# Performance work log

Hardware: AMD Instinct MI355X
Metric: run time of the kernel (lower is better)

The kernel has to match this reference:

```python
import jax, jax.numpy as jnp
import numpy as np

B, S, F = 2, 2048, 2048
H, D = 16, 128  # F == H * D


def setup_inputs() -> dict:
    key = jax.random.key(0)
    k1, k2, k3 = jax.random.split(key, 3)
    x = jax.random.normal(k1, (B, S, F), dtype=jnp.float32)
    # causal attention mask, broadcast over batch and heads
    mask = jnp.tril(jnp.ones((S, S), dtype=bool))[None, None, :, :]
    init_std = 0.02
    c_attn_kernel = jax.random.normal(k2, (F, 3 * F), dtype=jnp.float32) * init_std
    c_attn_bias = jnp.zeros((3 * F,), dtype=jnp.float32)
    c_proj_kernel = jax.random.normal(k3, (F, F), dtype=jnp.float32) * init_std
    c_proj_bias = jnp.zeros((F,), dtype=jnp.float32)
    return {
        "x": x,
        "mask": mask,
        "c_attn_kernel": c_attn_kernel,
        "c_attn_bias": c_attn_bias,
        "c_proj_kernel": c_proj_kernel,
        "c_proj_bias": c_proj_bias,
    }


def reference(x, mask, c_attn_kernel, c_attn_bias, c_proj_kernel, c_proj_bias):
    dtype = x.dtype
    # fused QKV projection: [B,S,F] @ [F,3F] -> [B,S,3F]
    hidden = jnp.einsum('bsf,fe->bse', x, c_attn_kernel) + c_attn_bias
    q, k, v = jnp.split(hidden, 3, axis=-1)
    split = lambda t: t.reshape(t.shape[:-1] + (H, D))  # [B,S,H,D]
    q, k, v = split(q), split(k), split(v)
    q = q / jnp.sqrt(jnp.asarray(D, dtype))
    scores = jnp.einsum('bqhd,bkhd->bhqk', q, k)  # [B,H,S,S]
    big_neg = jnp.finfo(dtype).min
    scores = jnp.where(mask[..., :S, :S], scores, big_neg)
    weights = jax.nn.softmax(scores, axis=-1)
    z = jnp.einsum('bhqk,bkhd->bqhd', weights, v)  # [B,S,H,D]
    merged = z.reshape(z.shape[:-2] + (F,))  # [B,S,F]
    out = jnp.einsum('bsf,fe->bse', merged, c_proj_kernel) + c_proj_bias
    return out
```

## Files before the change

### kernel.cpp

```cpp
#include <hip/hip_runtime.h>
#include <hip/hip_bf16.h>
#include <stdint.h>

typedef __attribute__((ext_vector_type(8))) __bf16 bf16x8;
typedef __attribute__((ext_vector_type(4))) __bf16 bf16x4;
typedef __attribute__((ext_vector_type(4))) float f32x4;

#define DEV __device__ __forceinline__

static constexpr int S = 2048, F = 2048, H = 16, D = 128;
static constexpr int KDIM = F;
static constexpr float QSCALE = 0.08838834764831845f;

DEV void gll16(const void* g, void* l) {
  __builtin_amdgcn_global_load_lds(
      (const __attribute__((address_space(1))) void*)g,
      (__attribute__((address_space(3))) void*)l, 16, 0, 0);
}

DEV f32x4 mfma16(bf16x8 a, bf16x8 b, f32x4 c) {
  return __builtin_amdgcn_mfma_f32_16x16x32_bf16(a, b, c, 0, 0, 0);
}

extern __shared__ char smem[];

__global__ void k_prep(const float* __restrict__ x, __bf16* __restrict__ xb,
                       const float* __restrict__ wa, __bf16* __restrict__ wat,
                       const float* __restrict__ wp, __bf16* __restrict__ wpt) {
  __shared__ float t[64][65];
  const int bid = blockIdx.x;
  if (bid < 8192) {
    int i = bid * 256 + threadIdx.x;
    float4 v = reinterpret_cast<const float4*>(x)[i];
    bf16x4 o = {(__bf16)v.x, (__bf16)v.y, (__bf16)v.z, (__bf16)v.w};
    reinterpret_cast<bf16x4*>(xb)[i] = o;
    return;
  }
  const float* in;
  __bf16* out;
  int rows, cols, c0, r0;
  if (bid < 11264) {
    int tb = bid - 8192;
    in = wa; out = wat; rows = 2048; cols = 6144;
    c0 = (tb % 96) * 64; r0 = (tb / 96) * 64;
  } else {
    int tb = bid - 11264;
    in = wp; out = wpt; rows = 2048; cols = 2048;
    c0 = (tb % 32) * 64; r0 = (tb / 32) * 64;
  }
  const int tx = threadIdx.x & 63, ty = threadIdx.x >> 6;
#pragma unroll
  for (int i = 0; i < 64; i += 4)
    t[ty + i][tx] = in[(size_t)(r0 + ty + i) * cols + c0 + tx];
  __syncthreads();
#pragma unroll
  for (int i = 0; i < 64; i += 4)
    out[(size_t)(c0 + ty + i) * rows + r0 + tx] = (__bf16)t[tx][ty + i];
}

template <int BM, int BN, int NBXL, int EPI>
__global__ __launch_bounds__(512, 1) void k_gp(
    const __bf16* __restrict__ A, const __bf16* __restrict__ Bt,
    const float* __restrict__ bias,
    __bf16* __restrict__ qo, __bf16* __restrict__ ko, __bf16* __restrict__ vo,
    float* __restrict__ fo) {
  constexpr int MF = BM / 32;
  constexpr int NF = BN / 64;
  constexpr int NH = NF / 2;
  constexpr int NLA = BM / 64;
  constexpr int NLB = BN / 64;
  constexpr int NL = NLA + NLB;
  constexpr int AOFF = BM * 128;
  constexpr int BUFSZ = (BM + BN) * 128;
  constexpr int NT = KDIM / 64;

  const int tid = threadIdx.x;
  const int lane = tid & 63, wid = tid >> 6;
  const int wm = wid >> 2, wn = wid & 3;
  const int ln = lane & 15, lm = lane >> 4;

  const int q8 = gridDim.x >> 3;
  const int lin = (blockIdx.x & 7) * q8 + (blockIdx.x >> 3);
  const int by = lin >> NBXL, bx = lin & ((1 << NBXL) - 1);
  const int mBase = by * BM, nBase = bx * BN;

  const int r0 = tid >> 3, cc = tid & 7;
  const int src0 = r0 * KDIM + ((cc ^ (r0 & 7)) << 3);
  const __bf16* Ab = A + (size_t)mBase * KDIM + src0;
  const __bf16* Bb = Bt + (size_t)nBase * KDIM + src0;
  const int dstBase = wid * 1024;

  auto stage = [&](char* buf, int t) {
    const __bf16* As = Ab + t * 64;
    const __bf16* Bs = Bb + t * 64;
#pragma unroll
    for (int j = 0; j < NLA; ++j)
      gll16(As + (size_t)j * 64 * KDIM, buf + j * 8192 + dstBase);
#pragma unroll
    for (int j = 0; j < NLB; ++j)
      gll16(Bs + (size_t)j * 64 * KDIM, buf + AOFF + j * 8192 + dstBase);
  };
  auto wait_nl = [&]() {
    if constexpr (NL == 4)       asm volatile("s_waitcnt vmcnt(4)" ::: "memory");
    else if constexpr (NL == 6)  asm volatile("s_waitcnt vmcnt(6)" ::: "memory");
    else if constexpr (NL == 8)  asm volatile("s_waitcnt vmcnt(8)" ::: "memory");
    else                         asm volatile("s_waitcnt vmcnt(10)" ::: "memory");
  };

  int rA[2], rB[2];
#pragma unroll
  for (int ks = 0; ks < 2; ++ks) {
    const int slot = (ks * 4 + lm) ^ (ln & 7);
    rA[ks] = (wm * (BM / 2) + ln) * 128 + slot * 16;
    rB[ks] = AOFF + (wn * (BN / 4) + ln) * 128 + slot * 16;
  }

  f32x4 acc[MF][NF] = {};

  stage(smem, 0);
  stage(smem + BUFSZ, 1);
  wait_nl();
  __builtin_amdgcn_s_barrier();
  __builtin_amdgcn_sched_barrier(0);

  for (int t = 0; t < NT; ++t) {
    char* cb = smem + (t & 1) * BUFSZ;
    bf16x8 a0[MF], a1[MF], b0[NF], b1[NF];

#pragma unroll
    for (int mi = 0; mi < MF; ++mi)
      a0[mi] = *reinterpret_cast<const bf16x8*>(cb + rA[0] + mi * 2048);
#pragma unroll
    for (int ni = 0; ni < NH; ++ni)
      b0[ni] = *reinterpret_cast<const bf16x8*>(cb + rB[0] + ni * 2048);
#pragma unroll
    for (int ni = NH; ni < NF; ++ni)
      b0[ni] = *reinterpret_cast<const bf16x8*>(cb + rB[0] + ni * 2048);

    __builtin_amdgcn_s_setprio(1);
#pragma unroll
    for (int ni = 0; ni < NH; ++ni)
#pragma unroll
      for (int mi = 0; mi < MF; ++mi)
        acc[mi][ni] = mfma16(a0[mi], b0[ni], acc[mi][ni]);
    __builtin_amdgcn_s_setprio(0);

#pragma unroll
    for (int mi = 0; mi < MF; ++mi)
      a1[mi] = *reinterpret_cast<const bf16x8*>(cb + rA[1] + mi * 2048);
#pragma unroll
    for (int ni = NH; ni < NF; ++ni)
      b1[ni] = *reinterpret_cast<const bf16x8*>(cb + rB[1] + ni * 2048);

    __builtin_amdgcn_s_setprio(1);
#pragma unroll
    for (int ni = NH; ni < NF; ++ni)
#pragma unroll
      for (int mi = 0; mi < MF; ++mi)
        acc[mi][ni] = mfma16(a0[mi], b0[ni], acc[mi][ni]);
    __builtin_amdgcn_s_setprio(0);

#pragma unroll
    for (int ni = 0; ni < NH; ++ni)
      b1[ni] = *reinterpret_cast<const bf16x8*>(cb + rB[1] + ni * 2048);

    __builtin_amdgcn_s_setprio(1);
#pragma unroll
    for (int ni = NH; ni < NF; ++ni)
#pragma unroll
      for (int mi = 0; mi < MF; ++mi)
        acc[mi][ni] = mfma16(a1[mi], b1[ni], acc[mi][ni]);
    __builtin_amdgcn_s_setprio(0);

    asm volatile("s_waitcnt lgkmcnt(0)" ::: "memory");
    __builtin_amdgcn_s_barrier();
    __builtin_amdgcn_sched_barrier(0);
    if (t + 2 < NT) stage(cb, t + 2);

    __builtin_amdgcn_s_setprio(1);
#pragma unroll
    for (int ni = 0; ni < NH; ++ni)
#pragma unroll
      for (int mi = 0; mi < MF; ++mi)
        acc[mi][ni] = mfma16(a1[mi], b1[ni], acc[mi][ni]);
    __builtin_amdgcn_s_setprio(0);

    if (t + 2 < NT) {
      wait_nl();
    } else if (t + 1 < NT) {
      asm volatile("s_waitcnt vmcnt(0)" ::: "memory");
    }
    if (t + 1 < NT) {
      __builtin_amdgcn_s_barrier();
      __builtin_amdgcn_sched_barrier(0);
    }
  }

  if (EPI == 0) {
#pragma unroll
    for (int mi = 0; mi < MF; ++mi) {
      const int grow = mBase + wm * (BM / 2) + mi * 16 + lm * 4;
      const int b = grow >> 11, s0 = grow & 2047;
#pragma unroll
      for (int ni = 0; ni < NF; ++ni) {
        const int gcol = nBase + wn * (BN / 4) + ni * 16 + ln;
        const float bv = bias[gcol];
        const int sec = gcol >> 11;
        const int h = (gcol >> 7) & 15, d = gcol & 127;
        const int bh = b * H + h;
        if (sec == 0) {
#pragma unroll
          for (int r = 0; r < 4; ++r)
            qo[((size_t)bh * S + s0 + r) * D + d] = (__bf16)((acc[mi][ni][r] + bv) * QSCALE);
        } else if (sec == 1) {
#pragma unroll
          for (int r = 0; r < 4; ++r)
            ko[((size_t)bh * S + s0 + r) * D + d] = (__bf16)(acc[mi][ni][r] + bv);
        } else {
          bf16x4 pv = {(__bf16)(acc[mi][ni][0] + bv), (__bf16)(acc[mi][ni][1] + bv),
                       (__bf16)(acc[mi][ni][2] + bv), (__bf16)(acc[mi][ni][3] + bv)};
          *reinterpret_cast<bf16x4*>(vo + ((size_t)bh * D + d) * S + s0) = pv;
        }
      }
    }
  } else {
#pragma unroll
    for (int mi = 0; mi < MF; ++mi) {
      const int grow = mBase + wm * (BM / 2) + mi * 16 + lm * 4;
#pragma unroll
      for (int ni = 0; ni < NF; ++ni) {
        const int gcol = nBase + wn * (BN / 4) + ni * 16 + ln;
        const float bv = bias[gcol];
#pragma unroll
        for (int r = 0; r < 4; ++r)
          fo[(size_t)(grow + r) * F + gcol] = acc[mi][ni][r] + bv;
      }
    }
  }
}

__global__ __launch_bounds__(256, 2) void k_attn(
    const __bf16* __restrict__ qb, const __bf16* __restrict__ kb,
    const __bf16* __restrict__ vtb, __bf16* __restrict__ zb) {
  const int lane = threadIdx.x & 63, w = threadIdx.x >> 6;
  const int lm = lane >> 4, ln = lane & 15;
  const int blk = blockIdx.x;
  const int u = blk & 255, v = blk >> 8;
  const int qt = v ? (u >> 4) : 15 - (u >> 4);
  const int bh = ((u & 15) << 1) | v;
  const int qw = qt * 128 + w * 32;

  const __bf16* qp = qb + (size_t)bh * S * D;
  const __bf16* kp = kb + (size_t)bh * S * D;
  const __bf16* vp = vtb + (size_t)bh * D * S;
  char* pw = smem + 65536 + w * 4096;

  int ksrc[4], kdst[4], vsrc[4], vdst[4];
#pragma unroll
  for (int j = 0; j < 4; ++j) {
    int c = (w * 4 + j) * 64 + lane;
    int kr = c >> 4, kps = (c & 15) ^ (kr & 7);
    ksrc[j] = kr * D + kps * 8;
    kdst[j] = (w * 4 + j) * 1024;
    int vr = c >> 3, vps = (c & 7) ^ (vr & 7);
    vsrc[j] = vr * S + vps * 8;
    vdst[j] = 16384 + (w * 4 + j) * 1024;
  }
  auto stage = [&](int kt) {
    char* buf = smem + (kt & 1) * 32768;
    const int kv = kt * 64;
#pragma unroll
    for (int j = 0; j < 4; ++j) gll16(kp + (size_t)kv * D + ksrc[j], buf + kdst[j]);
#pragma unroll
    for (int j = 0; j < 4; ++j) gll16(vp + kv + vsrc[j], buf + vdst[j]);
  };

  bf16x8 qf[2][4];
#pragma unroll
  for (int mi = 0; mi < 2; ++mi)
#pragma unroll
    for (int kf = 0; kf < 4; ++kf)
      qf[mi][kf] = *reinterpret_cast<const bf16x8*>(qp + (qw + mi * 16 + ln) * D + kf * 32 + lm * 8);

  f32x4 Oa[2][8] = {};
  float mrow[2][4], lrow[2][4];
#pragma unroll
  for (int mi = 0; mi < 2; ++mi)
#pragma unroll
    for (int r = 0; r < 4; ++r) { mrow[mi][r] = -3.0e38f; lrow[mi][r] = 0.0f; }

  const int ktEnd = 2 * qt + 1;

  stage(0);
  stage(1);
  asm volatile("s_waitcnt vmcnt(8)" ::: "memory");
  __builtin_amdgcn_s_barrier();
  __builtin_amdgcn_sched_barrier(0);

  for (int kt = 0; kt <= ktEnd; ++kt) {
    const int kv0 = kt * 64;
    const int cur = kt & 1;
    const char* Kb = smem + cur * 32768;
    const char* Vb = Kb + 16384;

    if (kv0 <= qw + 31) {
      const bool diag = (kv0 + 63 > qw);

      f32x4 sacc[2][4] = {};
#pragma unroll
      for (int kf = 0; kf < 4; ++kf) {
        bf16x8 kfr[4];
#pragma unroll
        for (int ni = 0; ni < 4; ++ni) {
          int row = ni * 16 + ln;
          int ch = (kf * 4 + lm) ^ (row & 7);
          kfr[ni] = *reinterpret_cast<const bf16x8*>(Kb + row * 256 + ch * 16);
        }
        __builtin_amdgcn_s_setprio(1);
#pragma unroll
        for (int mi = 0; mi < 2; ++mi)
#pragma unroll
          for (int ni = 0; ni < 4; ++ni)
            sacc[mi][ni] = mfma16(qf[mi][kf], kfr[ni], sacc[mi][ni]);
        __builtin_amdgcn_s_setprio(0);
      }

      if (diag) {
#pragma unroll
        for (int ni = 0; ni < 4; ++ni) {
          int c = kv0 + ni * 16 + ln;
#pragma unroll
          for (int mi = 0; mi < 2; ++mi) {
            int q0r = qw + mi * 16 + lm * 4;
#pragma unroll
            for (int r = 0; r < 4; ++r)
              if (c > q0r + r) sacc[mi][ni][r] = -1e30f;
          }
        }
      }

      float lmax[2][4];
      bool big = false;
#pragma unroll
      for (int mi = 0; mi < 2; ++mi)
#pragma unroll
        for (int r = 0; r < 4; ++r) {
          float m4 = fmaxf(fmaxf(sacc[mi][0][r], sacc[mi][1][r]),
                           fmaxf(sacc[mi][2][r], sacc[mi][3][r]));
          lmax[mi][r] = m4;
          big = big || (m4 > mrow[mi][r] + 8.0f);
        }
      if (__any((int)big)) {
#pragma unroll
        for (int mi = 0; mi < 2; ++mi)
#pragma unroll
          for (int r = 0; r < 4; ++r) {
            float mx = lmax[mi][r];
            mx = fmaxf(mx, __shfl_xor(mx, 1, 64));
            mx = fmaxf(mx, __shfl_xor(mx, 2, 64));
            mx = fmaxf(mx, __shfl_xor(mx, 4, 64));
            mx = fmaxf(mx, __shfl_xor(mx, 8, 64));
            float mnew = fmaxf(mrow[mi][r], mx);
            float corr = __expf(mrow[mi][r] - mnew);
            mrow[mi][r] = mnew;
            lrow[mi][r] *= corr;
#pragma unroll
            for (int ni = 0; ni < 8; ++ni) Oa[mi][ni][r] *= corr;
          }
      }
#pragma unroll
      for (int mi = 0; mi < 2; ++mi)
#pragma unroll
        for (int r = 0; r < 4; ++r) {
          float rs = 0.0f;
#pragma unroll
          for (int ni = 0; ni < 4; ++ni) {
            float p = __expf(sacc[mi][ni][r] - mrow[mi][r]);
            sacc[mi][ni][r] = p;
            rs += p;
          }
          lrow[mi][r] += rs;
        }

#pragma unroll
      for (int mi = 0; mi < 2; ++mi)
#pragma unroll
        for (int ni = 0; ni < 4; ++ni)
#pragma unroll
          for (int r = 0; r < 4; ++r) {
            int row = mi * 16 + lm * 4 + r;
            int bo = (row * 128 + (ni * 16 + ln) * 2) ^ ((row & 7) << 4);
            *reinterpret_cast<__bf16*>(pw + bo) = (__bf16)sacc[mi][ni][r];
          }

      asm volatile("s_waitcnt lgkmcnt(0)" ::: "memory");
      __builtin_amdgcn_sched_barrier(0);

#pragma unroll
      for (int kf = 0; kf < 2; ++kf) {
        bf16x8 pfr[2], vfr[8];
#pragma unroll
        for (int mi = 0; mi < 2; ++mi) {
          int row = mi * 16 + ln;
          int ch = (kf * 4 + lm) ^ (row & 7);
          pfr[mi] = *reinterpret_cast<const bf16x8*>(pw + row * 128 + ch * 16);
        }
#pragma unroll
        for (int ni = 0; ni < 8; ++ni) {
          int row = ni * 16 + ln;
          int ch = (kf * 4 + lm) ^ (row & 7);
          vfr[ni] = *reinterpret_cast<const bf16x8*>(Vb + row * 128 + ch * 16);
        }
        __builtin_amdgcn_s_setprio(1);
#pragma unroll
        for (int mi = 0; mi < 2; ++mi)
#pragma unroll
          for (int ni = 0; ni < 8; ++ni)
            Oa[mi][ni] = mfma16(pfr[mi], vfr[ni], Oa[mi][ni]);
        __builtin_amdgcn_s_setprio(0);
      }
    }

    asm volatile("s_waitcnt lgkmcnt(0)" ::: "memory");
    __builtin_amdgcn_s_barrier();
    __builtin_amdgcn_sched_barrier(0);
    if (kt + 2 <= ktEnd) stage(kt + 2);
    if (kt + 1 <= ktEnd) {
      if (kt + 2 <= ktEnd)
        asm volatile("s_waitcnt vmcnt(8)" ::: "memory");
      else
        asm volatile("s_waitcnt vmcnt(0)" ::: "memory");
      __builtin_amdgcn_s_barrier();
      __builtin_amdgcn_sched_barrier(0);
    }
  }

#pragma unroll
  for (int mi = 0; mi < 2; ++mi)
#pragma unroll
    for (int r = 0; r < 4; ++r) {
      float ls = lrow[mi][r];
      ls += __shfl_xor(ls, 1, 64);
      ls += __shfl_xor(ls, 2, 64);
      ls += __shfl_xor(ls, 4, 64);
      ls += __shfl_xor(ls, 8, 64);
      lrow[mi][r] = 1.0f / ls;
    }
  const int b = bh >> 4, h = bh & 15;
#pragma unroll
  for (int mi = 0; mi < 2; ++mi)
#pragma unroll
    for (int ni = 0; ni < 8; ++ni) {
      int d = ni * 16 + ln;
#pragma unroll
      for (int r = 0; r < 4; ++r) {
        int qrow = qw + mi * 16 + lm * 4 + r;
        zb[(size_t)(b * S + qrow) * F + h * D + d] = (__bf16)(Oa[mi][ni][r] * lrow[mi][r]);
      }
    }
}

extern "C" void kernel_launch(void* const* d_in, const int* in_sizes, int n_in,
                              void* d_out, int out_size, void* d_ws, size_t ws_size,
                              hipStream_t stream) {
  const float* x = (const float*)d_in[0];
  const float* w_attn = (const float*)d_in[2];
  const float* b_attn = (const float*)d_in[3];
  const float* w_proj = (const float*)d_in[4];
  const float* b_proj = (const float*)d_in[5];
  float* out = (float*)d_out;

  char* ws = (char*)d_ws;
  __bf16* xb    = (__bf16*)(ws + 0);
  __bf16* wqkv  = (__bf16*)(ws + 16777216);
  __bf16* wpro  = (__bf16*)(ws + 41943040);
  __bf16* qb    = (__bf16*)(ws + 50331648);
  __bf16* kb    = (__bf16*)(ws + 67108864);
  __bf16* vtb   = (__bf16*)(ws + 83886080);
  __bf16* zb    = xb;

  (void)hipFuncSetAttribute((const void*)k_gp<128, 384, 4, 0>,
                            hipFuncAttributeMaxDynamicSharedMemorySize, 131072);
  (void)hipFuncSetAttribute((const void*)k_gp<128, 256, 3, 1>,
                            hipFuncAttributeMaxDynamicSharedMemorySize, 98304);
  (void)hipFuncSetAttribute((const void*)k_attn,
                            hipFuncAttributeMaxDynamicSharedMemorySize, 81920);

  k_prep<<<12288, 256, 0, stream>>>(x, xb, w_attn, wqkv, w_proj, wpro);
  k_gp<128, 384, 4, 0><<<512, 512, 131072, stream>>>(xb, wqkv, b_attn, qb, kb, vtb, nullptr);
  k_attn<<<512, 256, 81920, stream>>>(qb, kb, vtb, zb);
  k_gp<128, 256, 3, 1><<<256, 512, 98304, stream>>>(zb, wpro, b_proj, nullptr, nullptr, nullptr, out);
}
```

Before: 237.1 us.

## Rewrite QKV GEMM main loop as eight-phase barrier-interleaved ping-pong schedule

```diff
diff --git a/kernel.cpp b/kernel.cpp
--- a/kernel.cpp
+++ b/kernel.cpp
@@ -23,6 +23,10 @@
 }
 
 extern __shared__ char smem[];
+
+#define QBAR()  __builtin_amdgcn_s_barrier()
+#define QLGKM() asm volatile("s_waitcnt lgkmcnt(0)" ::: "memory")
+#define QSCB()  __builtin_amdgcn_sched_barrier(0)
 
 __global__ void k_prep(const float* __restrict__ x, __bf16* __restrict__ xb,
                        const float* __restrict__ wa, __bf16* __restrict__ wat,
@@ -58,30 +62,169 @@
     out[(size_t)(c0 + ty + i) * rows + r0 + tx] = (__bf16)t[tx][ty + i];
 }
 
-template <int BM, int BN, int NBXL, int EPI>
-__global__ __launch_bounds__(512, 1) void k_gp(
+__global__ __launch_bounds__(512, 1) void k_qkv8p(
     const __bf16* __restrict__ A, const __bf16* __restrict__ Bt,
     const float* __restrict__ bias,
-    __bf16* __restrict__ qo, __bf16* __restrict__ ko, __bf16* __restrict__ vo,
-    float* __restrict__ fo) {
-  constexpr int MF = BM / 32;
-  constexpr int NF = BN / 64;
-  constexpr int NH = NF / 2;
-  constexpr int NLA = BM / 64;
-  constexpr int NLB = BN / 64;
-  constexpr int NL = NLA + NLB;
-  constexpr int AOFF = BM * 128;
-  constexpr int BUFSZ = (BM + BN) * 128;
-  constexpr int NT = KDIM / 64;
-
+    __bf16* __restrict__ qo, __bf16* __restrict__ ko, __bf16* __restrict__ vo) {
+  constexpr int NT = 32;
   const int tid = threadIdx.x;
   const int lane = tid & 63, wid = tid >> 6;
   const int wm = wid >> 2, wn = wid & 3;
   const int ln = lane & 15, lm = lane >> 4;
 
-  const int q8 = gridDim.x >> 3;
-  const int lin = (blockIdx.x & 7) * q8 + (blockIdx.x >> 3);
-  const int by = lin >> NBXL, bx = lin & ((1 << NBXL) - 1);
+  const int lin = (blockIdx.x & 7) * 64 + (blockIdx.x >> 3);
+  const int by = lin >> 4, bx = lin & 15;
+  const int mBase = by * 128, nBase = bx * 384;
+
+  const int r0 = tid >> 3, cc = tid & 7;
+  const int src0 = r0 * KDIM + ((cc ^ (r0 & 7)) << 3);
+  const __bf16* Ab = A + (size_t)mBase * KDIM + src0;
+  const __bf16* Bb = Bt + (size_t)nBase * KDIM + src0;
+  const int sDst = wid * 1024;
+
+  auto stA2 = [&](int t) {
+    char* d = smem + (t & 1) * 65536 + sDst;
+    const __bf16* s = Ab + t * 64;
+    gll16(s, d);
+    gll16(s + (size_t)64 * KDIM, d + 8192);
+  };
+  auto stB2 = [&](int t, int j) {
+    char* d = smem + (t & 1) * 65536 + 16384 + j * 8192 + sDst;
+    const __bf16* s = Bb + (size_t)j * 64 * KDIM + t * 64;
+    gll16(s, d);
+    gll16(s + (size_t)64 * KDIM, d + 8192);
+  };
+
+  int rA[2], rB[2];
+#pragma unroll
+  for (int ks = 0; ks < 2; ++ks) {
+    const int slot = (ks * 4 + lm) ^ (ln & 7);
+    rA[ks] = (wm * 64 + ln) * 128 + slot * 16;
+    rB[ks] = 16384 + (wn * 96 + ln) * 128 + slot * 16;
+  }
+  auto rdA = [&](bf16x8 (&a)[4], const char* cb, int ks) {
+#pragma unroll
+    for (int mi = 0; mi < 4; ++mi)
+      a[mi] = *reinterpret_cast<const bf16x8*>(cb + rA[ks] + mi * 2048);
+  };
+  auto rdBh = [&](bf16x8 (&b)[3], const char* cb, int ks, int h) {
+#pragma unroll
+    for (int k = 0; k < 3; ++k)
+      b[k] = *reinterpret_cast<const bf16x8*>(cb + rB[ks] + (h * 3 + k) * 2048);
+  };
+
+  f32x4 acc[4][6] = {};
+  auto mm = [&](const bf16x8 (&a)[4], const bf16x8 (&b)[3], int h) {
+#pragma unroll
+    for (int k = 0; k < 3; ++k)
+#pragma unroll
+      for (int mi = 0; mi < 4; ++mi)
+        acc[mi][h * 3 + k] = mfma16(a[mi], b[k], acc[mi][h * 3 + k]);
+  };
+
+  stA2(0); stB2(0, 0); stB2(0, 2); stB2(0, 4); stA2(1);
+  asm volatile("s_waitcnt vmcnt(2)" ::: "memory");
+  QBAR(); QSCB();
+
+  for (int i = 0; i < 16; ++i) {
+    const char* L = smem;
+    const char* R = smem + 65536;
+    const int tR = 2 * i + 1, tN = 2 * i + 2, tN1 = 2 * i + 3;
+    const bool last = (i == 15);
+    bf16x8 a[4], b[3];
+
+    rdA(a, L, 0); rdBh(b, L, 0, 0);
+    stB2(tR, 0);
+    QBAR(); QLGKM(); QSCB();
+    __builtin_amdgcn_s_setprio(1); mm(a, b, 0); __builtin_amdgcn_s_setprio(0);
+    QBAR(); QSCB();
+    rdBh(b, L, 0, 1);
+    stB2(tR, 2);
+    QBAR(); QLGKM(); QSCB();
+    __builtin_amdgcn_s_setprio(1); mm(a, b, 1); __builtin_amdgcn_s_setprio(0);
+    QBAR(); QSCB();
+    rdA(a, L, 1); rdBh(b, L, 1, 1);
+    stB2(tR, 4);
+    QBAR(); QLGKM(); QSCB();
+    __builtin_amdgcn_s_setprio(1); mm(a, b, 1); __builtin_amdgcn_s_setprio(0);
+    QBAR(); QSCB();
+    rdBh(b, L, 1, 0);
+    if (!last) stA2(tN);
+    QBAR(); QLGKM(); QSCB();
+    __builtin_amdgcn_s_setprio(1); mm(a, b, 0); __builtin_amdgcn_s_setprio(0);
+    if (last) asm volatile("s_waitcnt vmcnt(0)" ::: "memory");
+    else      asm volatile("s_waitcnt vmcnt(2)" ::: "memory");
+    QBAR(); QSCB();
+
+    rdA(a, R, 0); rdBh(b, R, 0, 0);
+    if (!last) stB2(tN, 0);
+    QBAR(); QLGKM(); QSCB();
+    __builtin_amdgcn_s_setprio(1); mm(a, b, 0); __builtin_amdgcn_s_setprio(0);
+    QBAR(); QSCB();
+    rdBh(b, R, 0, 1);
+    if (!last) stB2(tN, 2);
+    QBAR(); QLGKM(); QSCB();
+    __builtin_amdgcn_s_setprio(1); mm(a, b, 1); __builtin_amdgcn_s_setprio(0);
+    QBAR(); QSCB();
+    rdA(a, R, 1); rdBh(b, R, 1, 1);
+    if (!last) stB2(tN, 4);
+    QBAR(); QLGKM(); QSCB();
+    __builtin_amdgcn_s_setprio(1); mm(a, b, 1); __builtin_amdgcn_s_setprio(0);
+    QBAR(); QSCB();
+    rdBh(b, R, 1, 0);
+    if (tN1 < NT) stA2(tN1);
+    QBAR(); QLGKM(); QSCB();
+    __builtin_amdgcn_s_setprio(1); mm(a, b, 0); __builtin_amdgcn_s_setprio(0);
+    if (!last) {
+      asm volatile("s_waitcnt vmcnt(2)" ::: "memory");
+      QBAR(); QSCB();
+    }
+  }
+
+#pragma unroll
+  for (int mi = 0; mi < 4; ++mi) {
+    const int grow = mBase + wm * 64 + mi * 16 + lm * 4;
+    const int b = grow >> 11, s0 = grow & 2047;
+#pragma unroll
+    for (int ni = 0; ni < 6; ++ni) {
+      const int gcol = nBase + wn * 96 + ni * 16 + ln;
+      const float bv = bias[gcol];
+      const int sec = gcol >> 11;
+      const int h = (gcol >> 7) & 15, d = gcol & 127;
+      const int bh = b * H + h;
+      if (sec == 0) {
+#pragma unroll
+        for (int r = 0; r < 4; ++r)
+          qo[((size_t)bh * S + s0 + r) * D + d] = (__bf16)((acc[mi][ni][r] + bv) * QSCALE);
+      } else if (sec == 1) {
+#pragma unroll
+        for (int r = 0; r < 4; ++r)
+          ko[((size_t)bh * S + s0 + r) * D + d] = (__bf16)(acc[mi][ni][r] + bv);
+      } else {
+        bf16x4 pv = {(__bf16)(acc[mi][ni][0] + bv), (__bf16)(acc[mi][ni][1] + bv),
+                     (__bf16)(acc[mi][ni][2] + bv), (__bf16)(acc[mi][ni][3] + bv)};
+        *reinterpret_cast<bf16x4*>(vo + ((size_t)bh * D + d) * S + s0) = pv;
+      }
+    }
+  }
+}
+
+__global__ __launch_bounds__(512, 1) void k_proj(
+    const __bf16* __restrict__ A, const __bf16* __restrict__ Bt,
+    const float* __restrict__ bias, float* __restrict__ fo) {
+  constexpr int BM = 128, BN = 256;
+  constexpr int MF = 4, NF = 4, NH = 2;
+  constexpr int AOFF = BM * 128;
+  constexpr int BUFSZ = (BM + BN) * 128;
+  constexpr int NT = KDIM / 64;
+
+  const int tid = threadIdx.x;
+  const int lane = tid & 63, wid = tid >> 6;
+  const int wm = wid >> 2, wn = wid & 3;
+  const int ln = lane & 15, lm = lane >> 4;
+
+  const int lin = (blockIdx.x & 7) * 32 + (blockIdx.x >> 3);
+  const int by = lin >> 3, bx = lin & 7;
   const int mBase = by * BM, nBase = bx * BN;
 
   const int r0 = tid >> 3, cc = tid & 7;
@@ -94,34 +237,27 @@
     const __bf16* As = Ab + t * 64;
     const __bf16* Bs = Bb + t * 64;
 #pragma unroll
-    for (int j = 0; j < NLA; ++j)
+    for (int j = 0; j < 2; ++j)
       gll16(As + (size_t)j * 64 * KDIM, buf + j * 8192 + dstBase);
 #pragma unroll
-    for (int j = 0; j < NLB; ++j)
+    for (int j = 0; j < 4; ++j)
       gll16(Bs + (size_t)j * 64 * KDIM, buf + AOFF + j * 8192 + dstBase);
-  };
-  auto wait_nl = [&]() {
-    if constexpr (NL == 4)       asm volatile("s_waitcnt vmcnt(4)" ::: "memory");
-    else if constexpr (NL == 6)  asm volatile("s_waitcnt vmcnt(6)" ::: "memory");
-    else if constexpr (NL == 8)  asm volatile("s_waitcnt vmcnt(8)" ::: "memory");
-    else                         asm volatile("s_waitcnt vmcnt(10)" ::: "memory");
   };
 
   int rA[2], rB[2];
 #pragma unroll
   for (int ks = 0; ks < 2; ++ks) {
     const int slot = (ks * 4 + lm) ^ (ln & 7);
-    rA[ks] = (wm * (BM / 2) + ln) * 128 + slot * 16;
-    rB[ks] = AOFF + (wn * (BN / 4) + ln) * 128 + slot * 16;
+    rA[ks] = (wm * 64 + ln) * 128 + slot * 16;
+    rB[ks] = AOFF + (wn * 64 + ln) * 128 + slot * 16;
   }
 
   f32x4 acc[MF][NF] = {};
 
   stage(smem, 0);
   stage(smem + BUFSZ, 1);
-  wait_nl();
-  __builtin_amdgcn_s_barrier();
-  __builtin_amdgcn_sched_barrier(0);
+  asm volatile("s_waitcnt vmcnt(6)" ::: "memory");
+  QBAR(); QSCB();
 
   for (int t = 0; t < NT; ++t) {
     char* cb = smem + (t & 1) * BUFSZ;
@@ -131,10 +267,7 @@
     for (int mi = 0; mi < MF; ++mi)
       a0[mi] = *reinterpret_cast<const bf16x8*>(cb + rA[0] + mi * 2048);
 #pragma unroll
-    for (int ni = 0; ni < NH; ++ni)
-      b0[ni] = *reinterpret_cast<const bf16x8*>(cb + rB[0] + ni * 2048);
-#pragma unroll
-    for (int ni = NH; ni < NF; ++ni)
+    for (int ni = 0; ni < NF; ++ni)
       b0[ni] = *reinterpret_cast<const bf16x8*>(cb + rB[0] + ni * 2048);
 
     __builtin_amdgcn_s_setprio(1);
@@ -172,9 +305,8 @@
         acc[mi][ni] = mfma16(a1[mi], b1[ni], acc[mi][ni]);
     __builtin_amdgcn_s_setprio(0);
 
-    asm volatile("s_waitcnt lgkmcnt(0)" ::: "memory");
-    __builtin_amdgcn_s_barrier();
-    __builtin_amdgcn_sched_barrier(0);
+    QLGKM();
+    QBAR(); QSCB();
     if (t + 2 < NT) stage(cb, t + 2);
 
     __builtin_amdgcn_s_setprio(1);
@@ -186,55 +318,25 @@
     __builtin_amdgcn_s_setprio(0);
 
     if (t + 2 < NT) {
-      wait_nl();
+      asm volatile("s_waitcnt vmcnt(6)" ::: "memory");
     } else if (t + 1 < NT) {
       asm volatile("s_waitcnt vmcnt(0)" ::: "memory");
     }
     if (t + 1 < NT) {
-      __builtin_amdgcn_s_barrier();
-      __builtin_amdgcn_sched_barrier(0);
-    }
-  }
-
-  if (EPI == 0) {
-#pragma unroll
-    for (int mi = 0; mi < MF; ++mi) {
-      const int grow = mBase + wm * (BM / 2) + mi * 16 + lm * 4;
-      const int b = grow >> 11, s0 = grow & 2047;
-#pragma unroll
-      for (int ni = 0; ni < NF; ++ni) {
-        const int gcol = nBase + wn * (BN / 4) + ni * 16 + ln;
-        const float bv = bias[gcol];
-        const int sec = gcol >> 11;
-        const int h = (gcol >> 7) & 15, d = gcol & 127;
-        const int bh = b * H + h;
-        if (sec == 0) {
-#pragma unroll
-          for (int r = 0; r < 4; ++r)
-            qo[((size_t)bh * S + s0 + r) * D + d] = (__bf16)((acc[mi][ni][r] + bv) * QSCALE);
-        } else if (sec == 1) {
-#pragma unroll
-          for (int r = 0; r < 4; ++r)
-            ko[((size_t)bh * S + s0 + r) * D + d] = (__bf16)(acc[mi][ni][r] + bv);
-        } else {
-          bf16x4 pv = {(__bf16)(acc[mi][ni][0] + bv), (__bf16)(acc[mi][ni][1] + bv),
-                       (__bf16)(acc[mi][ni][2] + bv), (__bf16)(acc[mi][ni][3] + bv)};
-          *reinterpret_cast<bf16x4*>(vo + ((size_t)bh * D + d) * S + s0) = pv;
-        }
-      }
-    }
-  } else {
-#pragma unroll
-    for (int mi = 0; mi < MF; ++mi) {
-      const int grow = mBase + wm * (BM / 2) + mi * 16 + lm * 4;
-#pragma unroll
-      for (int ni = 0; ni < NF; ++ni) {
-        const int gcol = nBase + wn * (BN / 4) + ni * 16 + ln;
-        const float bv = bias[gcol];
-#pragma unroll
-        for (int r = 0; r < 4; ++r)
-          fo[(size_t)(grow + r) * F + gcol] = acc[mi][ni][r] + bv;
-      }
+      QBAR(); QSCB();
+    }
+  }
+
+#pragma unroll
+  for (int mi = 0; mi < MF; ++mi) {
+    const int grow = mBase + wm * 64 + mi * 16 + lm * 4;
+#pragma unroll
+    for (int ni = 0; ni < NF; ++ni) {
+      const int gcol = nBase + wn * 64 + ni * 16 + ln;
+      const float bv = bias[gcol];
+#pragma unroll
+      for (int r = 0; r < 4; ++r)
+        fo[(size_t)(grow + r) * F + gcol] = acc[mi][ni][r] + bv;
     }
   }
 }
@@ -294,8 +396,7 @@
   stage(0);
   stage(1);
   asm volatile("s_waitcnt vmcnt(8)" ::: "memory");
-  __builtin_amdgcn_s_barrier();
-  __builtin_amdgcn_sched_barrier(0);
+  QBAR(); QSCB();
 
   for (int kt = 0; kt <= ktEnd; ++kt) {
     const int kv0 = kt * 64;
@@ -393,8 +494,7 @@
             *reinterpret_cast<__bf16*>(pw + bo) = (__bf16)sacc[mi][ni][r];
           }
 
-      asm volatile("s_waitcnt lgkmcnt(0)" ::: "memory");
-      __builtin_amdgcn_sched_barrier(0);
+      QLGKM(); QSCB();
 
 #pragma unroll
       for (int kf = 0; kf < 2; ++kf) {
@@ -422,16 +522,14 @@
     }
 
     asm volatile("s_waitcnt lgkmcnt(0)" ::: "memory");
-    __builtin_amdgcn_s_barrier();
-    __builtin_amdgcn_sched_barrier(0);
+    QBAR(); QSCB();
     if (kt + 2 <= ktEnd) stage(kt + 2);
     if (kt + 1 <= ktEnd) {
       if (kt + 2 <= ktEnd)
         asm volatile("s_waitcnt vmcnt(8)" ::: "memory");
       else
         asm volatile("s_waitcnt vmcnt(0)" ::: "memory");
-      __builtin_amdgcn_s_barrier();
-      __builtin_amdgcn_sched_barrier(0);
+      QBAR(); QSCB();
     }
   }
 
@@ -479,15 +577,15 @@
   __bf16* vtb   = (__bf16*)(ws + 83886080);
   __bf16* zb    = xb;
 
-  (void)hipFuncSetAttribute((const void*)k_gp<128, 384, 4, 0>,
+  (void)hipFuncSetAttribute((const void*)k_qkv8p,
                             hipFuncAttributeMaxDynamicSharedMemorySize, 131072);
-  (void)hipFuncSetAttribute((const void*)k_gp<128, 256, 3, 1>,
+  (void)hipFuncSetAttribute((const void*)k_proj,
                             hipFuncAttributeMaxDynamicSharedMemorySize, 98304);
   (void)hipFuncSetAttribute((const void*)k_attn,
                             hipFuncAttributeMaxDynamicSharedMemorySize, 81920);
 
   k_prep<<<12288, 256, 0, stream>>>(x, xb, w_attn, wqkv, w_proj, wpro);
-  k_gp<128, 384, 4, 0><<<512, 512, 131072, stream>>>(xb, wqkv, b_attn, qb, kb, vtb, nullptr);
+  k_qkv8p<<<512, 512, 131072, stream>>>(xb, wqkv, b_attn, qb, kb, vtb);
   k_attn<<<512, 256, 81920, stream>>>(qb, kb, vtb, zb);
-  k_gp<128, 256, 3, 1><<<256, 512, 98304, stream>>>(zb, wpro, b_proj, nullptr, nullptr, nullptr, out);
-}
+  k_proj<<<256, 512, 98304, stream>>>(zb, wpro, b_proj, out);
+}
```

New measurement: 235.4 us. Within noise of the previous version (-0.7%).
